# Kernel tuning notes

Hardware: AMD Instinct MI355X
Metric: run time of the kernel (lower is better)

Reference implementation:

```python
import jax, jax.numpy as jnp
import numpy as np

B, S, D, H = 2, 2048, 1024, 16
HD = D // H  # head_dim = 64
ROPE_BASE = 10000.0
NEG_MIN = jnp.finfo(jnp.float32).min


def _rope_cos_sin(seq_len, head_dim):
    inv_freq = 1.0 / (ROPE_BASE ** (jnp.arange(0, head_dim, 2, dtype=jnp.float32) / head_dim))
    t = jnp.arange(seq_len, dtype=jnp.float32)
    freqs = jnp.einsum('i,j->ij', t, inv_freq)           # [S, HD/2]
    emb = jnp.concatenate([freqs, freqs], axis=-1)        # [S, HD]
    return jnp.cos(emb), jnp.sin(emb)


def _rotate_half(x):
    x1, x2 = jnp.split(x, 2, axis=-1)
    return jnp.concatenate([-x2, x1], axis=-1)


def setup_inputs() -> dict:
    key = jax.random.key(0)
    ks = jax.random.split(key, 5)
    sc = 0.02
    hidden_states = jax.random.normal(ks[0], (B, S, D), dtype=jnp.float32)
    wq = jax.random.normal(ks[1], (D, D), dtype=jnp.float32) * sc
    wk = jax.random.normal(ks[2], (D, D), dtype=jnp.float32) * sc
    wv = jax.random.normal(ks[3], (D, D), dtype=jnp.float32) * sc
    wo = jax.random.normal(ks[4], (D, D), dtype=jnp.float32) * sc
    # additive causal mask [B,1,S,S]: 0 on/below diagonal, large negative above
    causal = jnp.tril(jnp.ones((S, S), dtype=jnp.bool_))
    attention_mask = jnp.where(causal, 0.0, NEG_MIN)[None, None, :, :].astype(jnp.float32)
    attention_mask = jnp.broadcast_to(attention_mask, (B, 1, S, S))
    position_ids = jnp.broadcast_to(jnp.arange(S, dtype=jnp.int32)[None, :], (B, S))
    return {"hidden_states": hidden_states, "attention_mask": attention_mask,
            "wq": wq, "wk": wk, "wv": wv, "wo": wo, "position_ids": position_ids}


def reference(hidden_states, attention_mask, wq, wk, wv, wo, position_ids):
    bsz, q_len, _ = hidden_states.shape

    def shape_heads(x):
        return x.reshape(bsz, q_len, H, HD).transpose(0, 2, 1, 3)  # [B,H,S,HD]

    q = shape_heads(hidden_states @ wq)
    k = shape_heads(hidden_states @ wk)
    v = shape_heads(hidden_states @ wv)

    cos, sin = _rope_cos_sin(q_len, HD)                   # [S, HD]
    cos = cos[position_ids][:, None, :, :]                # [B,1,S,HD]
    sin = sin[position_ids][:, None, :, :]
    q = q * cos + _rotate_half(q) * sin
    k = k * cos + _rotate_half(k) * sin

    scores = jnp.einsum('bhqd,bhkd->bhqk', q, k) / jnp.sqrt(jnp.float32(HD))
    scores = jnp.maximum(scores + attention_mask, NEG_MIN)
    attn = jax.nn.softmax(scores, axis=-1)
    out = jnp.einsum('bhqk,bhkd->bhqd', attn, v)          # [B,H,S,HD]
    out = out.transpose(0, 2, 1, 3).reshape(bsz, q_len, D)
    return out @ wo
```

## Files before the change

### kernel.cpp

```cpp
#include <hip/hip_runtime.h>
#include <hip/hip_bf16.h>

#define B_ 2
#define S_ 2048
#define D_ 1024
#define H_ 16
#define HD_ 64

typedef unsigned short u16;
typedef __attribute__((ext_vector_type(8))) short short8;
typedef __attribute__((ext_vector_type(4))) float f32x4;

#if __has_builtin(__builtin_amdgcn_exp2f)
#define EXP2F(x) __builtin_amdgcn_exp2f(x)
#else
#define EXP2F(x) exp2f(x)
#endif

__device__ __forceinline__ u16 f2bf(float f) {
  union { float f; unsigned u; } v; v.f = f;
  unsigned r = v.u + 0x7fffu + ((v.u >> 16) & 1u);
  return (u16)(r >> 16);
}
__device__ __forceinline__ unsigned pkbf(float a, float b) {
  union { __hip_bfloat162 h; unsigned u; } v;
  v.h = __float22bfloat162_rn(float2{a, b});
  return v.u;
}
__device__ __forceinline__ void gload_lds16(const u16* g, u16* l) {
  __builtin_amdgcn_global_load_lds((const __attribute__((address_space(1))) void*)g,
                                   (__attribute__((address_space(3))) void*)l, 16, 0, 0);
}

__global__ __launch_bounds__(256) void prep_kernel(const float* __restrict__ hs,
                                                   const float* __restrict__ W0,
                                                   const float* __restrict__ W1,
                                                   const float* __restrict__ W2,
                                                   const float* __restrict__ W3,
                                                   u16* __restrict__ Xb,
                                                   u16* __restrict__ WT) {
  __shared__ float T[64][65];
  if (blockIdx.z == 4) {
    const int base = (blockIdx.y * 16 + blockIdx.x) * 4096 + threadIdx.x;
#pragma unroll 4
    for (int i = 0; i < 16; ++i) {
      const int idx = base + i * 256;
      const float4 v = ((const float4*)hs)[idx];
      ushort4 o;
      o.x = f2bf(v.x); o.y = f2bf(v.y); o.z = f2bf(v.z); o.w = f2bf(v.w);
      ((ushort4*)Xb)[idx] = o;
    }
    return;
  }
  const float* Wz[4] = {W0, W1, W2, W3};
  const float* W = Wz[blockIdx.z];
  u16* dst = WT + (size_t)blockIdx.z * (1024 * 1024);
  const int nb = blockIdx.x * 64, kb = blockIdx.y * 64;
  const int t = threadIdx.x;
  const int r = t >> 2, c4 = (t & 3) * 16;
#pragma unroll
  for (int i = 0; i < 4; ++i) {
    float4 v = *(const float4*)&W[(kb + r) * D_ + nb + c4 + i * 4];
    T[r][c4 + i * 4 + 0] = v.x;
    T[r][c4 + i * 4 + 1] = v.y;
    T[r][c4 + i * 4 + 2] = v.z;
    T[r][c4 + i * 4 + 3] = v.w;
  }
  __syncthreads();
#pragma unroll
  for (int i = 0; i < 4; ++i) {
    ushort4 o;
    o.x = f2bf(T[c4 + i * 4 + 0][r]);
    o.y = f2bf(T[c4 + i * 4 + 1][r]);
    o.z = f2bf(T[c4 + i * 4 + 2][r]);
    o.w = f2bf(T[c4 + i * 4 + 3][r]);
    *(ushort4*)&dst[(nb + r) * D_ + kb + c4 + i * 4] = o;
  }
}

template <int BN, int MODE>
__global__ __launch_bounds__(256) void gemm_kernel(const u16* __restrict__ A,
                                                   const u16* __restrict__ BT,
                                                   float* __restrict__ out0,
                                                   u16* __restrict__ oQ,
                                                   u16* __restrict__ oK,
                                                   u16* __restrict__ oV,
                                                   const int* __restrict__ posarr) {
  constexpr int K = D_;
  constexpr int BK = 32;
  constexpr int NSTEP = K / BK;
  constexpr int NT = BN / 32;
  constexpr int NBR = (BN * BK) / 2048;
  constexpr int ABANK = 128 * BK;
  constexpr int BBANK = BN * BK;
  constexpr int BUFSZ = ABANK + BBANK;
  constexpr int EPIU = (MODE == 1) ? 128 * 136 : 0;
  constexpr int SMU = (3 * BUFSZ > EPIU) ? 3 * BUFSZ : EPIU;
  __shared__ u16 smem[SMU];

  const int t = threadIdx.x, lane = t & 63, w = t >> 6;
  const int l15 = lane & 15, quad = lane >> 4;
  const int flat = blockIdx.x;
  const int xcd = flat & 7, j = flat >> 3;
  const int m0 = ((xcd << 2) + (j & 3)) * 128;
  const int n0 = (j >> 2) * BN;
  const int wm = (w >> 1) * 64, wn = (w & 1) * (BN / 2);

  f32x4 acc[4][NT];
#pragma unroll
  for (int mt = 0; mt < 4; ++mt)
#pragma unroll
    for (int nt = 0; nt < NT; ++nt) acc[mt][nt] = (f32x4){0.f, 0.f, 0.f, 0.f};

  const u16* agp[2]; int adst[2];
  const u16* bgp[NBR]; int bdst[NBR];
#pragma unroll
  for (int jj = 0; jj < 2; ++jj) {
    const int slot = jj * 256 + w * 64 + lane;
    const int row = slot >> 2, c = slot & 3, q = c ^ ((row >> 1) & 3);
    agp[jj] = A + (size_t)(m0 + row) * K + q * 8;
    adst[jj] = (jj * 256 + w * 64) * 8;
  }
#pragma unroll
  for (int jj = 0; jj < NBR; ++jj) {
    const int slot = jj * 256 + w * 64 + lane;
    const int row = slot >> 2, c = slot & 3, q = c ^ ((row >> 1) & 3);
    bgp[jj] = BT + (size_t)(n0 + row) * K + q * 8;
    bdst[jj] = ABANK + (jj * 256 + w * 64) * 8;
  }

  auto stage = [&](int k0, int buf) {
    u16* base = smem + buf * BUFSZ;
#pragma unroll
    for (int jj = 0; jj < 2; ++jj) gload_lds16(agp[jj] + k0, base + adst[jj]);
#pragma unroll
    for (int jj = 0; jj < NBR; ++jj) gload_lds16(bgp[jj] + k0, base + bdst[jj]);
  };

  int afo[4], bfo[NT];
#pragma unroll
  for (int mt = 0; mt < 4; ++mt) {
    const int row = wm + mt * 16 + l15;
    afo[mt] = row * BK + (quad ^ ((row >> 1) & 3)) * 8;
  }
#pragma unroll
  for (int nt = 0; nt < NT; ++nt) {
    const int col = wn + nt * 16 + l15;
    bfo[nt] = ABANK + col * BK + (quad ^ ((col >> 1) & 3)) * 8;
  }

  auto compute = [&](int buf) {
    const u16* base = smem + buf * BUFSZ;
    short8 af[4], bf[NT];
#pragma unroll
    for (int mt = 0; mt < 4; ++mt) af[mt] = *(const short8*)&base[afo[mt]];
#pragma unroll
    for (int nt = 0; nt < NT; ++nt) bf[nt] = *(const short8*)&base[bfo[nt]];
#pragma unroll
    for (int mt = 0; mt < 4; ++mt)
#pragma unroll
      for (int nt = 0; nt < NT; ++nt)
        acc[mt][nt] = __builtin_amdgcn_mfma_f32_16x16x32_bf16(af[mt], bf[nt], acc[mt][nt], 0, 0, 0);
  };

  stage(0, 0);
  stage(BK, 1);
  int bc = 0, bs = 2;
#pragma unroll 1
  for (int it = 0; it < NSTEP - 2; ++it) {
    if constexpr (MODE == 1) asm volatile("s_waitcnt vmcnt(4)" ::: "memory");
    else                     asm volatile("s_waitcnt vmcnt(3)" ::: "memory");
    __builtin_amdgcn_s_barrier();
    __builtin_amdgcn_sched_barrier(0);
    stage((it + 2) * BK, bs);
    compute(bc);
    bc = bc == 2 ? 0 : bc + 1;
    bs = bs == 2 ? 0 : bs + 1;
  }
  if constexpr (MODE == 1) asm volatile("s_waitcnt vmcnt(4)" ::: "memory");
  else                     asm volatile("s_waitcnt vmcnt(3)" ::: "memory");
  __builtin_amdgcn_s_barrier();
  __builtin_amdgcn_sched_barrier(0);
  compute(bc);
  bc = bc == 2 ? 0 : bc + 1;
  asm volatile("s_waitcnt vmcnt(0)" ::: "memory");
  __builtin_amdgcn_s_barrier();
  __builtin_amdgcn_sched_barrier(0);
  compute(bc);

  if (MODE == 0) {
#pragma unroll
    for (int mt = 0; mt < 4; ++mt) {
      const int row0 = m0 + wm + mt * 16 + quad * 4;
#pragma unroll
      for (int nt = 0; nt < NT; ++nt) {
        const int col = n0 + wn + nt * 16 + l15;
#pragma unroll
        for (int r = 0; r < 4; ++r) out0[(size_t)(row0 + r) * 1024 + col] = acc[mt][nt][r];
      }
    }
  } else {
    const int widx = n0 >> 10;
    if (widx == 2) {
      __syncthreads();
      u16* Epi = smem;
#pragma unroll
      for (int nt = 0; nt < NT; ++nt) {
        const int col = wn + nt * 16 + l15;
#pragma unroll
        for (int mt = 0; mt < 4; ++mt) {
          const int row0 = wm + mt * 16 + quad * 4;
          uint2 pk;
          pk.x = pkbf(acc[mt][nt][0], acc[mt][nt][1]);
          pk.y = pkbf(acc[mt][nt][2], acc[mt][nt][3]);
          *(uint2*)&Epi[col * 136 + row0] = pk;
        }
      }
      __syncthreads();
      const int col = t >> 1, half = t & 1;
      const int cc = (n0 + col) & 1023;
      const int h = cc >> 6, d = cc & 63;
      const int bb = m0 >> 11;
      const int s0 = (m0 & (S_ - 1)) + half * 64;
      u16* gp = oV + ((((size_t)(bb * H_ + h) * HD_ + d)) << 11) + s0;
#pragma unroll
      for (int i = 0; i < 8; ++i)
        ((uint4*)gp)[i] = *(const uint4*)&Epi[col * 136 + half * 64 + i * 8];
    } else {
      u16* dst = (widx == 0) ? oQ : oK;
      const float scale = (widx == 0) ? 0.18033688011f : 1.0f;
      float invf[2];
      invf[0] = exp2f(-0.41524101186f * (float)l15);
      invf[1] = exp2f(-0.41524101186f * (float)(16 + l15));
      __syncthreads();
      u16* Epi = smem;
#pragma unroll
      for (int mt = 0; mt < 4; ++mt) {
        const int lrow0 = wm + mt * 16 + quad * 4;
#pragma unroll
        for (int r = 0; r < 4; ++r) {
          const int rw = m0 + lrow0 + r;
          const int b = rw >> 11, s = rw & (S_ - 1);
          const float pos = (float)posarr[b * S_ + s];
#pragma unroll
          for (int nt2 = 0; nt2 < 2; ++nt2) {
            float sn, c;
            __sincosf(pos * invf[nt2], &sn, &c);
            const float x1 = acc[mt][nt2][r], x2 = acc[mt][nt2 + 2][r];
            const int d = nt2 * 16 + l15;
            Epi[(lrow0 + r) * 136 + wn + d] = f2bf((x1 * c - x2 * sn) * scale);
            Epi[(lrow0 + r) * 136 + wn + d + 32] = f2bf((x2 * c + x1 * sn) * scale);
          }
        }
      }
      __syncthreads();
      const int bb = m0 >> 11, s0 = m0 & (S_ - 1);
      const int sl = t >> 1, d0 = (t & 1) * 32;
#pragma unroll
      for (int hh = 0; hh < 2; ++hh) {
        const int h = ((n0 + hh * 64) & 1023) >> 6;
        u16* gp = dst + (((size_t)(bb * H_ + h) * S_ + s0 + sl) << 6) + d0;
#pragma unroll
        for (int k2 = 0; k2 < 4; ++k2)
          ((uint4*)gp)[k2] = *(const uint4*)&Epi[sl * 136 + hh * 64 + d0 + k2 * 8];
      }
    }
  }
}

__global__ __launch_bounds__(256, 2) void attn_kernel(const u16* __restrict__ Q,
                                                      const u16* __restrict__ Kx,
                                                      const u16* __restrict__ Vt,
                                                      u16* __restrict__ AO) {
  __shared__ u16 Ks[2][2][512 * 8];
  __shared__ u16 Vs[2][2][512 * 8];
  __shared__ u16 Pw[4][2][128 * 8];
  const int t = threadIdx.x;
  const int lane = t & 63, w = t >> 6;
  const int l15 = lane & 15, quad = lane >> 4;
  const int idx = blockIdx.x;
  const int pr = (idx >> 3) & 15;
  const int bh = (idx & 7) | ((idx >> 7) << 3);
  const int qtA = pr, qtB = 31 - pr;
  const u16* qp = Q + bh * (S_ * HD_);
  const u16* kp = Kx + bh * (S_ * HD_);
  const u16* vp = Vt + bh * (HD_ * S_);
  const int wq16 = w * 16;
  const int q_loA = qtA * 64 + wq16;
  const int q_loB = qtB * 64 + wq16;

  int srow[2], sq[2];
#pragma unroll
  for (int jj = 0; jj < 2; ++jj) {
    int slot = w * 128 + jj * 64 + lane;
    srow[jj] = slot >> 3;
    sq[jj] = (slot & 7) ^ (srow[jj] & 7);
  }
  auto stageT = [&](int kt, int buf, int tt) {
#pragma unroll
    for (int jj = 0; jj < 2; ++jj)
      gload_lds16(kp + (size_t)(kt * 64 + srow[jj]) * 64 + sq[jj] * 8,
                  &Ks[buf][tt][(w * 128 + jj * 64) * 8]);
#pragma unroll
    for (int jj = 0; jj < 2; ++jj)
      gload_lds16(vp + (size_t)srow[jj] * S_ + kt * 64 + sq[jj] * 8,
                  &Vs[buf][tt][(w * 128 + jj * 64) * 8]);
  };
  auto stageGroup = [&](int g, int buf, int ktmax) {
    const int kt0 = g * 2;
    stageT(kt0, buf, 0);
    if (kt0 + 1 <= ktmax) stageT(kt0 + 1, buf, 1);
  };

  short8 qfA[2], qfB[2];
#pragma unroll
  for (int kc = 0; kc < 2; ++kc) {
    qfA[kc] = *(const short8*)&qp[(q_loA + l15) * HD_ + kc * 32 + quad * 8];
    qfB[kc] = *(const short8*)&qp[(q_loB + l15) * HD_ + kc * 32 + quad * 8];
  }

  f32x4 oA[4], oB[4];
  f32x4 lsA = (f32x4){0.f, 0.f, 0.f, 0.f}, lsB = (f32x4){0.f, 0.f, 0.f, 0.f};
  float mA = -INFINITY, mB = -INFINITY;
#pragma unroll
  for (int i = 0; i < 4; ++i) {
    oA[i] = (f32x4){0.f, 0.f, 0.f, 0.f};
    oB[i] = (f32x4){0.f, 0.f, 0.f, 0.f};
  }
  const short8 ones = {0x3F80, 0x3F80, 0x3F80, 0x3F80, 0x3F80, 0x3F80, 0x3F80, 0x3F80};

  auto chainStep = [&](bool diag, const short8* qf, const short8* kf, const short8* vf,
                       f32x4* o, float& m_, f32x4& ls, u16* pwb) {
    f32x4 sa[4];
#pragma unroll
    for (int i = 0; i < 4; ++i) sa[i] = (f32x4){0.f, 0.f, 0.f, 0.f};
    __builtin_amdgcn_s_setprio(1);
#pragma unroll
    for (int kc = 0; kc < 2; ++kc)
#pragma unroll
      for (int nt = 0; nt < 4; ++nt)
        sa[nt] = __builtin_amdgcn_mfma_f32_16x16x32_bf16(kf[kc * 4 + nt], qf[kc], sa[nt], 0, 0, 0);
    __builtin_amdgcn_s_setprio(0);
    if (diag) {
#pragma unroll
      for (int nt = 0; nt < 4; ++nt)
#pragma unroll
        for (int r = 0; r < 4; ++r)
          if (nt * 16 + quad * 4 + r > wq16 + l15) sa[nt][r] = -INFINITY;
    }
    float mq[4];
#pragma unroll
    for (int nt = 0; nt < 4; ++nt)
      mq[nt] = fmaxf(fmaxf(sa[nt][0], sa[nt][1]), fmaxf(sa[nt][2], sa[nt][3]));
    float mx = fmaxf(fmaxf(mq[0], mq[1]), fmaxf(mq[2], mq[3]));
    mx = fmaxf(mx, __shfl_xor(mx, 16));
    mx = fmaxf(mx, __shfl_xor(mx, 32));
    if (!__all(mx <= m_)) {
      const float mn = fmaxf(m_, mx);
      const float alpha = EXP2F(m_ - mn);
      m_ = mn;
#pragma unroll
      for (int dt = 0; dt < 4; ++dt)
#pragma unroll
        for (int r = 0; r < 4; ++r) o[dt][r] *= alpha;
      ls *= alpha;
    }
#pragma unroll
    for (int nt = 0; nt < 4; ++nt) {
      const int q = nt * 2 + (quad >> 1);
      uint2 pk;
      pk.x = pkbf(EXP2F(sa[nt][0] - m_), EXP2F(sa[nt][1] - m_));
      pk.y = pkbf(EXP2F(sa[nt][2] - m_), EXP2F(sa[nt][3] - m_));
      *(uint2*)&pwb[(l15 * 8 + (q ^ (l15 & 7))) * 8 + (quad & 1) * 4] = pk;
    }
    __builtin_amdgcn_s_setprio(1);
#pragma unroll
    for (int kc = 0; kc < 2; ++kc) {
      short8 pf = *(const short8*)&pwb[(l15 * 8 + (((kc * 4) + quad) ^ (l15 & 7))) * 8];
#pragma unroll
      for (int dt = 0; dt < 4; ++dt)
        o[dt] = __builtin_amdgcn_mfma_f32_16x16x32_bf16(vf[dt * 2 + kc], pf, o[dt], 0, 0, 0);
      ls = __builtin_amdgcn_mfma_f32_16x16x32_bf16(ones, pf, ls, 0, 0, 0);
    }
    __builtin_amdgcn_s_setprio(0);
  };

  auto loadFrags = [&](int buf, int tt, short8* kf, short8* vf) {
#pragma unroll
    for (int kc = 0; kc < 2; ++kc)
#pragma unroll
      for (int nt = 0; nt < 4; ++nt) {
        const int row = nt * 16 + l15;
        kf[kc * 4 + nt] =
            *(const short8*)&Ks[buf][tt][(row * 8 + ((kc * 4 + quad) ^ (row & 7))) * 8];
      }
#pragma unroll
    for (int dt = 0; dt < 4; ++dt)
#pragma unroll
      for (int kc = 0; kc < 2; ++kc) {
        const int row = dt * 16 + l15;
        vf[dt * 2 + kc] =
            *(const short8*)&Vs[buf][tt][(row * 8 + ((kc * 4 + quad) ^ (row & 7))) * 8];
      }
  };

  const int ktmax = qtB;
  const int ngroups = (ktmax + 2) >> 1;
  short8 kf[8], vf[8];
  stageGroup(0, 0, ktmax);
#pragma unroll 1
  for (int g = 0; g < ngroups; ++g) {
    __syncthreads();
    if (g + 1 < ngroups) stageGroup(g + 1, (g + 1) & 1, ktmax);
    const int buf = g & 1;
    const int kt0 = 2 * g;
    loadFrags(buf, 0, kf, vf);
    chainStep(kt0 == qtB, qfB, kf, vf, oB, mB, lsB, &Pw[w][1][0]);
    if (kt0 <= qtA) chainStep(kt0 == qtA, qfA, kf, vf, oA, mA, lsA, &Pw[w][0][0]);
    if (kt0 + 1 <= ktmax) {
      loadFrags(buf, 1, kf, vf);
      chainStep(kt0 + 1 == qtB, qfB, kf, vf, oB, mB, lsB, &Pw[w][1][0]);
      if (kt0 + 1 <= qtA) chainStep(kt0 + 1 == qtA, qfA, kf, vf, oA, mA, lsA, &Pw[w][0][0]);
    }
  }

  const int b = bh >> 4, h = bh & 15;
  const float liA = 1.0f / lsA[0], liB = 1.0f / lsB[0];
  const size_t baseA = ((size_t)(b * S_ + q_loA + l15)) * D_ + h * HD_;
  const size_t baseB = ((size_t)(b * S_ + q_loB + l15)) * D_ + h * HD_;
#pragma unroll
  for (int dt = 0; dt < 4; ++dt)
#pragma unroll
    for (int rr = 0; rr < 2; ++rr) {
      *(unsigned*)&AO[baseA + dt * 16 + quad * 4 + rr * 2] =
          pkbf(oA[dt][rr * 2] * liA, oA[dt][rr * 2 + 1] * liA);
      *(unsigned*)&AO[baseB + dt * 16 + quad * 4 + rr * 2] =
          pkbf(oB[dt][rr * 2] * liB, oB[dt][rr * 2 + 1] * liB);
    }
}

extern "C" void kernel_launch(void* const* d_in, const int* in_sizes, int n_in,
                              void* d_out, int out_size, void* d_ws, size_t ws_size,
                              hipStream_t stream) {
  const float* hs = (const float*)d_in[0];
  const float* wq = (const float*)d_in[2];
  const float* wk = (const float*)d_in[3];
  const float* wv = (const float*)d_in[4];
  const float* wo = (const float*)d_in[5];
  const int* pos = (const int*)d_in[6];
  float* out = (float*)d_out;

  char* ws = (char*)d_ws;
  const size_t MB = (size_t)1 << 20;
  u16* Xb = (u16*)(ws);
  u16* WT = (u16*)(ws + 8 * MB);
  u16* Qh = (u16*)(ws + 16 * MB);
  u16* Kh = (u16*)(ws + 24 * MB);
  u16* Vt = (u16*)(ws + 32 * MB);
  u16* AO = (u16*)(ws + 40 * MB);

  prep_kernel<<<dim3(16, 16, 5), 256, 0, stream>>>(hs, wq, wk, wv, wo, Xb, WT);

  gemm_kernel<128, 1><<<768, 256, 0, stream>>>(Xb, WT, nullptr, Qh, Kh, Vt, pos);

  attn_kernel<<<512, 256, 0, stream>>>(Qh, Kh, Vt, AO);

  gemm_kernel<64, 0><<<512, 256, 0, stream>>>(AO, WT + 3 * 1024 * 1024, out,
                                              nullptr, nullptr, nullptr, nullptr);
}
```

Before: 203.4 us.

## Process two key tiles per softmax update in attention chain step

The per-tile chain step is replaced by a fused step that computes scores for both key tiles of a staged group, does one max and rescale across both, then runs both PV products. This halves the online-softmax reductions, cross-lane shuffles and rescales, and gives the scheduler more independent MFMAs. The cost is higher register pressure from doubled K/V fragments and score tiles. The K/V fragments are also reloaded from LDS separately for the A and B query chains instead of being shared, and the setprio hints are dropped.

```diff
diff --git a/kernel.cpp b/kernel.cpp
--- a/kernel.cpp
+++ b/kernel.cpp
@@ -31,6 +31,8 @@
   __builtin_amdgcn_global_load_lds((const __attribute__((address_space(1))) void*)g,
                                    (__attribute__((address_space(3))) void*)l, 16, 0, 0);
 }
+
+template <int N> struct IC { static constexpr int v = N; };
 
 __global__ __launch_bounds__(256) void prep_kernel(const float* __restrict__ hs,
                                                    const float* __restrict__ W0,
@@ -329,30 +331,44 @@
   }
   const short8 ones = {0x3F80, 0x3F80, 0x3F80, 0x3F80, 0x3F80, 0x3F80, 0x3F80, 0x3F80};
 
-  auto chainStep = [&](bool diag, const short8* qf, const short8* kf, const short8* vf,
-                       f32x4* o, float& m_, f32x4& ls, u16* pwb) {
-    f32x4 sa[4];
-#pragma unroll
-    for (int i = 0; i < 4; ++i) sa[i] = (f32x4){0.f, 0.f, 0.f, 0.f};
-    __builtin_amdgcn_s_setprio(1);
-#pragma unroll
-    for (int kc = 0; kc < 2; ++kc)
-#pragma unroll
-      for (int nt = 0; nt < 4; ++nt)
-        sa[nt] = __builtin_amdgcn_mfma_f32_16x16x32_bf16(kf[kc * 4 + nt], qf[kc], sa[nt], 0, 0, 0);
-    __builtin_amdgcn_s_setprio(0);
-    if (diag) {
-#pragma unroll
-      for (int nt = 0; nt < 4; ++nt)
-#pragma unroll
-        for (int r = 0; r < 4; ++r)
-          if (nt * 16 + quad * 4 + r > wq16 + l15) sa[nt][r] = -INFINITY;
-    }
-    float mq[4];
-#pragma unroll
-    for (int nt = 0; nt < 4; ++nt)
-      mq[nt] = fmaxf(fmaxf(sa[nt][0], sa[nt][1]), fmaxf(sa[nt][2], sa[nt][3]));
-    float mx = fmaxf(fmaxf(mq[0], mq[1]), fmaxf(mq[2], mq[3]));
+  auto fusedStep = [&](auto NTT, int kt0, int qt_, const short8* qf,
+                       f32x4* o, float& m_, f32x4& ls, int buf) {
+    constexpr int N2 = decltype(NTT)::v;
+    short8 kf[N2][8];
+#pragma unroll
+    for (int tt = 0; tt < N2; ++tt)
+#pragma unroll
+      for (int kc = 0; kc < 2; ++kc)
+#pragma unroll
+        for (int nt = 0; nt < 4; ++nt) {
+          const int row = nt * 16 + l15;
+          kf[tt][kc * 4 + nt] =
+              *(const short8*)&Ks[buf][tt][(row * 8 + ((kc * 4 + quad) ^ (row & 7))) * 8];
+        }
+    f32x4 sa[N2 * 4];
+#pragma unroll
+    for (int i = 0; i < N2 * 4; ++i) sa[i] = (f32x4){0.f, 0.f, 0.f, 0.f};
+#pragma unroll
+    for (int tt = 0; tt < N2; ++tt)
+#pragma unroll
+      for (int kc = 0; kc < 2; ++kc)
+#pragma unroll
+        for (int nt = 0; nt < 4; ++nt)
+          sa[tt * 4 + nt] = __builtin_amdgcn_mfma_f32_16x16x32_bf16(
+              kf[tt][kc * 4 + nt], qf[kc], sa[tt * 4 + nt], 0, 0, 0);
+#pragma unroll
+    for (int tt = 0; tt < N2; ++tt)
+      if (kt0 + tt == qt_) {
+#pragma unroll
+        for (int nt = 0; nt < 4; ++nt)
+#pragma unroll
+          for (int r = 0; r < 4; ++r)
+            if (nt * 16 + quad * 4 + r > wq16 + l15) sa[tt * 4 + nt][r] = -INFINITY;
+      }
+    float mx = -INFINITY;
+#pragma unroll
+    for (int i = 0; i < N2 * 4; ++i)
+      mx = fmaxf(mx, fmaxf(fmaxf(sa[i][0], sa[i][1]), fmaxf(sa[i][2], sa[i][3])));
     mx = fmaxf(mx, __shfl_xor(mx, 16));
     mx = fmaxf(mx, __shfl_xor(mx, 32));
     if (!__all(mx <= m_)) {
@@ -366,47 +382,41 @@
       ls *= alpha;
     }
 #pragma unroll
-    for (int nt = 0; nt < 4; ++nt) {
-      const int q = nt * 2 + (quad >> 1);
-      uint2 pk;
-      pk.x = pkbf(EXP2F(sa[nt][0] - m_), EXP2F(sa[nt][1] - m_));
-      pk.y = pkbf(EXP2F(sa[nt][2] - m_), EXP2F(sa[nt][3] - m_));
-      *(uint2*)&pwb[(l15 * 8 + (q ^ (l15 & 7))) * 8 + (quad & 1) * 4] = pk;
-    }
-    __builtin_amdgcn_s_setprio(1);
-#pragma unroll
-    for (int kc = 0; kc < 2; ++kc) {
-      short8 pf = *(const short8*)&pwb[(l15 * 8 + (((kc * 4) + quad) ^ (l15 & 7))) * 8];
+    for (int tt = 0; tt < N2; ++tt)
+#pragma unroll
+      for (int nt = 0; nt < 4; ++nt) {
+        const int q = nt * 2 + (quad >> 1);
+        uint2 pk;
+        pk.x = pkbf(EXP2F(sa[tt * 4 + nt][0] - m_), EXP2F(sa[tt * 4 + nt][1] - m_));
+        pk.y = pkbf(EXP2F(sa[tt * 4 + nt][2] - m_), EXP2F(sa[tt * 4 + nt][3] - m_));
+        *(uint2*)&Pw[w][tt][(l15 * 8 + (q ^ (l15 & 7))) * 8 + (quad & 1) * 4] = pk;
+      }
+    short8 vf[N2][8];
+#pragma unroll
+    for (int tt = 0; tt < N2; ++tt)
 #pragma unroll
       for (int dt = 0; dt < 4; ++dt)
-        o[dt] = __builtin_amdgcn_mfma_f32_16x16x32_bf16(vf[dt * 2 + kc], pf, o[dt], 0, 0, 0);
-      ls = __builtin_amdgcn_mfma_f32_16x16x32_bf16(ones, pf, ls, 0, 0, 0);
-    }
-    __builtin_amdgcn_s_setprio(0);
-  };
-
-  auto loadFrags = [&](int buf, int tt, short8* kf, short8* vf) {
-#pragma unroll
-    for (int kc = 0; kc < 2; ++kc)
-#pragma unroll
-      for (int nt = 0; nt < 4; ++nt) {
-        const int row = nt * 16 + l15;
-        kf[kc * 4 + nt] =
-            *(const short8*)&Ks[buf][tt][(row * 8 + ((kc * 4 + quad) ^ (row & 7))) * 8];
-      }
-#pragma unroll
-    for (int dt = 0; dt < 4; ++dt)
+#pragma unroll
+        for (int kc = 0; kc < 2; ++kc) {
+          const int row = dt * 16 + l15;
+          vf[tt][dt * 2 + kc] =
+              *(const short8*)&Vs[buf][tt][(row * 8 + ((kc * 4 + quad) ^ (row & 7))) * 8];
+        }
+#pragma unroll
+    for (int tt = 0; tt < N2; ++tt)
 #pragma unroll
       for (int kc = 0; kc < 2; ++kc) {
-        const int row = dt * 16 + l15;
-        vf[dt * 2 + kc] =
-            *(const short8*)&Vs[buf][tt][(row * 8 + ((kc * 4 + quad) ^ (row & 7))) * 8];
+        short8 pf =
+            *(const short8*)&Pw[w][tt][(l15 * 8 + (((kc * 4) + quad) ^ (l15 & 7))) * 8];
+#pragma unroll
+        for (int dt = 0; dt < 4; ++dt)
+          o[dt] = __builtin_amdgcn_mfma_f32_16x16x32_bf16(vf[tt][dt * 2 + kc], pf, o[dt], 0, 0, 0);
+        ls = __builtin_amdgcn_mfma_f32_16x16x32_bf16(ones, pf, ls, 0, 0, 0);
       }
   };
 
   const int ktmax = qtB;
   const int ngroups = (ktmax + 2) >> 1;
-  short8 kf[8], vf[8];
   stageGroup(0, 0, ktmax);
 #pragma unroll 1
   for (int g = 0; g < ngroups; ++g) {
@@ -414,13 +424,11 @@
     if (g + 1 < ngroups) stageGroup(g + 1, (g + 1) & 1, ktmax);
     const int buf = g & 1;
     const int kt0 = 2 * g;
-    loadFrags(buf, 0, kf, vf);
-    chainStep(kt0 == qtB, qfB, kf, vf, oB, mB, lsB, &Pw[w][1][0]);
-    if (kt0 <= qtA) chainStep(kt0 == qtA, qfA, kf, vf, oA, mA, lsA, &Pw[w][0][0]);
-    if (kt0 + 1 <= ktmax) {
-      loadFrags(buf, 1, kf, vf);
-      chainStep(kt0 + 1 == qtB, qfB, kf, vf, oB, mB, lsB, &Pw[w][1][0]);
-      if (kt0 + 1 <= qtA) chainStep(kt0 + 1 == qtA, qfA, kf, vf, oA, mA, lsA, &Pw[w][0][0]);
+    if (kt0 + 1 <= qtB) fusedStep(IC<2>{}, kt0, qtB, qfB, oB, mB, lsB, buf);
+    else                fusedStep(IC<1>{}, kt0, qtB, qfB, oB, mB, lsB, buf);
+    if (kt0 <= qtA) {
+      if (kt0 + 1 <= qtA) fusedStep(IC<2>{}, kt0, qtA, qfA, oA, mA, lsA, buf);
+      else                fusedStep(IC<1>{}, kt0, qtA, qfA, oA, mA, lsA, buf);
     }
   }
 
```

After: 204.4 us. No clear change (+0.5%).
